# Kernel tuning notes

Measured on AMD Instinct MI355X. Metric: run time of the kernel, lower is better.

## Reference

```python
import jax, jax.numpy as jnp
import numpy as np

B, DIM, D_IN, HID, N_HID_EXTRA = 65536, 128, 64, 512, 2  # num_hidden_layers=3 -> 2 extra hidden linears
LOG_SCALE_CLAMP = 2.0


def _mlp(x, Win, bin_, Whid, bhid, Wout, bout):
    # torch nn.Linear: y = x @ W.T + b
    h = jax.nn.relu(x @ Win.T + bin_)
    for i in range(Whid.shape[0]):  # fixed small layer loop
        h = jax.nn.relu(h @ Whid[i].T + bhid[i])
    return h @ Wout.T + bout


def setup_inputs() -> dict:
    key = jax.random.key(0)
    ks = jax.random.split(key, 13)
    w = lambda k, shp: (jax.random.normal(k, shp, dtype=jnp.float32) * 0.05)
    d_out = DIM - D_IN
    return {
        "z": jax.random.normal(ks[0], (B, DIM), dtype=jnp.float32),
        "s_Win": w(ks[1], (HID, D_IN)),   "s_bin": jnp.zeros((HID,), jnp.float32),
        "s_Whid": w(ks[2], (N_HID_EXTRA, HID, HID)), "s_bhid": jnp.zeros((N_HID_EXTRA, HID), jnp.float32),
        "s_Wout": w(ks[3], (d_out, HID)), "s_bout": jnp.zeros((d_out,), jnp.float32),
        "t_Win": w(ks[4], (HID, D_IN)),   "t_bin": jnp.zeros((HID,), jnp.float32),
        "t_Whid": w(ks[5], (N_HID_EXTRA, HID, HID)), "t_bhid": jnp.zeros((N_HID_EXTRA, HID), jnp.float32),
        "t_Wout": w(ks[6], (d_out, HID)), "t_bout": jnp.zeros((d_out,), jnp.float32),
    }


def reference(z, s_Win, s_bin, s_Whid, s_bhid, s_Wout, s_bout,
              t_Win, t_bin, t_Whid, t_bhid, t_Wout, t_bout):
    # mask = first D_IN dims -> gather reduces to slicing
    z1 = z[:, :D_IN]   # (B, d_in)  passthrough half
    z2 = z[:, D_IN:]   # (B, d_out) transformed half
    log_s = jnp.clip(_mlp(z1, s_Win, s_bin, s_Whid, s_bhid, s_Wout, s_bout),
                     -LOG_SCALE_CLAMP, LOG_SCALE_CLAMP)
    t = _mlp(z1, t_Win, t_bin, t_Whid, t_bhid, t_Wout, t_bout)
    z2_out = z2 * jnp.exp(log_s) + t
    z_out = jnp.concatenate([z1, z2_out], axis=1)  # scatter back per mask
    log_det = log_s.sum(axis=-1)                   # (B,)
    return (z_out, log_det)
```

## Files before the change

kernel.cpp:

```cpp
#include <hip/hip_runtime.h>
#include <stdint.h>


#define NROWS 65536
#define RPB   128
#define NBLK  (NROWS / RPB)

#define OFF_S_WIN   0
#define OFF_S_WHID  32768
#define OFF_S_WOUT  557056
#define OFF_T_WIN   589824
#define OFF_T_WHID  622592
#define OFF_T_WOUT  1146880
#define W_ELEMS     1179648

typedef __attribute__((ext_vector_type(8)))  short short8;
typedef __attribute__((ext_vector_type(4)))  float f32x4;
typedef __attribute__((ext_vector_type(16))) float f32x16;

__device__ __forceinline__ uint32_t f2bf1(float f) {
  uint32_t u = __float_as_uint(f);
  return (u + 0x7fffu + ((u >> 16) & 1u)) >> 16;
}
__device__ __forceinline__ uint32_t pk2bf(float a, float b) {
  return f2bf1(a) | (f2bf1(b) << 16);
}

__global__ void cvt_weights(const float* __restrict__ sWin, const float* __restrict__ sWhid,
                            const float* __restrict__ sWout, const float* __restrict__ tWin,
                            const float* __restrict__ tWhid, const float* __restrict__ tWout,
                            uint16_t* __restrict__ wbf) {
  int g = blockIdx.x * blockDim.x + threadIdx.x;
  int e = g * 4;
  if (e >= W_ELEMS) return;
  const float* src; int off, base; bool k64;
  if      (e < OFF_S_WHID) { src = sWin;  off = e;              base = OFF_S_WIN;  k64 = true; }
  else if (e < OFF_S_WOUT) { src = sWhid; off = e - OFF_S_WHID; base = OFF_S_WHID; k64 = false; }
  else if (e < OFF_T_WIN)  { src = sWout; off = e - OFF_S_WOUT; base = OFF_S_WOUT; k64 = false; }
  else if (e < OFF_T_WHID) { src = tWin;  off = e - OFF_T_WIN;  base = OFF_T_WIN;  k64 = true; }
  else if (e < OFF_T_WOUT) { src = tWhid; off = e - OFF_T_WHID; base = OFF_T_WHID; k64 = false; }
  else                     { src = tWout; off = e - OFF_T_WOUT; base = OFF_T_WOUT; k64 = false; }
  int m, k, tsz;
  if (k64) { m = off >> 6; k = off & 63;  tsz = 2048;  }
  else     { m = off >> 9; k = off & 511; tsz = 16384; }
  int dest = base + (m >> 5) * tsz + (k >> 3) * 256 + (m & 31) * 8 + (k & 7);
  f32x4 v = *(const f32x4*)(src + off);
  uint2 r; r.x = pk2bf(v.x, v.y); r.y = pk2bf(v.z, v.w);
  *(uint2*)(wbf + dest) = r;
}

template<bool BF>
__device__ __forceinline__ short8 ldW(const uint16_t* __restrict__ wb,
                                      const float* __restrict__ wf, int pidx, int oidx) {
  if (BF) {
    return *(const short8*)(wb + pidx);
  } else {
    f32x4 x = *(const f32x4*)(wf + oidx);
    f32x4 y = *(const f32x4*)(wf + oidx + 4);
    short8 r;
    r[0] = (short)f2bf1(x.x); r[1] = (short)f2bf1(x.y);
    r[2] = (short)f2bf1(x.z); r[3] = (short)f2bf1(x.w);
    r[4] = (short)f2bf1(y.x); r[5] = (short)f2bf1(y.y);
    r[6] = (short)f2bf1(y.z); r[7] = (short)f2bf1(y.w);
    return r;
  }
}

#define MFMA32(a, b, c) __builtin_amdgcn_mfma_f32_32x32x16_bf16(a, b, c, 0, 0, 0)

__device__ __forceinline__ void store_h32(f32x16 acc[2][4], const float* __restrict__ bias,
                                          uint16_t* hdst, int wave, int lane) {
  const int l31 = lane & 31, lh = lane >> 5;
  __syncthreads();
  char* wp = (char*)hdst + wave * 16384 + l31 * 16 + lh * 8;
  #pragma unroll
  for (int nt = 0; nt < 2; ++nt) {
    #pragma unroll
    for (int q = 0; q < 4; ++q) {
      const int m0 = wave * 64 + nt * 32 + q * 8 + lh * 4;
      f32x4 bv = *(const f32x4*)(bias + m0);
      #pragma unroll
      for (int rt = 0; rt < 4; ++rt) {
        float v0 = acc[nt][rt][q * 4 + 0] + bv.x;
        float v1 = acc[nt][rt][q * 4 + 1] + bv.y;
        float v2 = acc[nt][rt][q * 4 + 2] + bv.z;
        float v3 = acc[nt][rt][q * 4 + 3] + bv.w;
        uint2 p;
        p.x = pk2bf(fmaxf(v0, 0.f), fmaxf(v1, 0.f));
        p.y = pk2bf(fmaxf(v2, 0.f), fmaxf(v3, 0.f));
        *(uint2*)(wp + nt * 8192 + q * 2048 + rt * 512) = p;
      }
    }
  }
  __syncthreads();
}

template<bool BF>
__device__ __forceinline__ void dense_in(
    const uint16_t* __restrict__ wb, const float* __restrict__ wf,
    const float* __restrict__ bias, const float* __restrict__ z, long rowbase,
    uint16_t* hdst, int wave, int lane) {
  const int l31 = lane & 31, lh = lane >> 5;
  f32x16 acc[2][4];
  #pragma unroll
  for (int i = 0; i < 2; ++i)
    #pragma unroll
    for (int j = 0; j < 4; ++j) acc[i][j] = (f32x16)0.f;
  #pragma unroll 1
  for (int ks = 0; ks < 4; ++ks) {
    short8 a0 = ldW<BF>(wb, wf, (wave * 2 + 0) * 2048 + (2 * ks + lh) * 256 + l31 * 8,
                        (wave * 64 + 0 + l31) * 64 + ks * 16 + lh * 8);
    short8 a1 = ldW<BF>(wb, wf, (wave * 2 + 1) * 2048 + (2 * ks + lh) * 256 + l31 * 8,
                        (wave * 64 + 32 + l31) * 64 + ks * 16 + lh * 8);
    #pragma unroll
    for (int rt = 0; rt < 4; ++rt) {
      const float* zp = z + (rowbase + rt * 32 + l31) * 128 + ks * 16 + lh * 8;
      f32x4 u = *(const f32x4*)zp;
      f32x4 v = *(const f32x4*)(zp + 4);
      short8 b;
      b[0] = (short)f2bf1(u.x); b[1] = (short)f2bf1(u.y);
      b[2] = (short)f2bf1(u.z); b[3] = (short)f2bf1(u.w);
      b[4] = (short)f2bf1(v.x); b[5] = (short)f2bf1(v.y);
      b[6] = (short)f2bf1(v.z); b[7] = (short)f2bf1(v.w);
      acc[0][rt] = MFMA32(a0, b, acc[0][rt]);
      acc[1][rt] = MFMA32(a1, b, acc[1][rt]);
    }
  }
  store_h32(acc, bias, hdst, wave, lane);
}

#define HSTEP(AC0, AC1, BC0, BC1, BC2, BC3, AN0, AN1, BN0, BN1, BN2, BN3, AOFF, BOFF) \
  AN0 = ldW<BF>(wb, wf, wpc + (AOFF),         woc + (AOFF) / 32);                     \
  AN1 = ldW<BF>(wb, wf, wpc + 16384 + (AOFF), woc + 16384 + (AOFF) / 32);             \
  BN0 = *(const short8*)(bc + (BOFF));                                                \
  BN1 = *(const short8*)(bc + (BOFF) + 512);                                          \
  BN2 = *(const short8*)(bc + (BOFF) + 1024);                                         \
  BN3 = *(const short8*)(bc + (BOFF) + 1536);                                         \
  __builtin_amdgcn_s_setprio(1);                                                      \
  acc[0][0] = MFMA32(AC0, BC0, acc[0][0]);                                            \
  acc[0][1] = MFMA32(AC0, BC1, acc[0][1]);                                            \
  acc[0][2] = MFMA32(AC0, BC2, acc[0][2]);                                            \
  acc[0][3] = MFMA32(AC0, BC3, acc[0][3]);                                            \
  acc[1][0] = MFMA32(AC1, BC0, acc[1][0]);                                            \
  acc[1][1] = MFMA32(AC1, BC1, acc[1][1]);                                            \
  acc[1][2] = MFMA32(AC1, BC2, acc[1][2]);                                            \
  acc[1][3] = MFMA32(AC1, BC3, acc[1][3]);                                            \
  __builtin_amdgcn_s_setprio(0);

template<bool BF>
__device__ __forceinline__ void dense_relu512(
    const uint16_t* __restrict__ wb, const float* __restrict__ wf,
    const float* __restrict__ bias, uint16_t* hbuf, int wave, int lane) {
  const int l31 = lane & 31, lh = lane >> 5;
  f32x16 acc[2][4];
  #pragma unroll
  for (int i = 0; i < 2; ++i)
    #pragma unroll
    for (int j = 0; j < 4; ++j) acc[i][j] = (f32x16)0.f;
  const int wbaseP = wave * 2 * 16384 + lh * 256 + l31 * 8;
  const int wbaseO = (wave * 64 + l31) * 512 + lh * 8;
  const char* bb = (const char*)hbuf + lh * 2048 + l31 * 16;

  short8 aC0, aC1, aN0, aN1, bC0, bC1, bC2, bC3, bN0, bN1, bN2, bN3;
  aC0 = ldW<BF>(wb, wf, wbaseP, wbaseO);
  aC1 = ldW<BF>(wb, wf, wbaseP + 16384, wbaseO + 16384);
  bC0 = *(const short8*)(bb);
  bC1 = *(const short8*)(bb + 512);
  bC2 = *(const short8*)(bb + 1024);
  bC3 = *(const short8*)(bb + 1536);

  #pragma unroll 1
  for (int c = 0; c < 7; ++c) {
    const int   wpc = wbaseP + c * 2048;
    const int   woc = wbaseO + c * 64;
    const char* bc  = bb + c * 16384;
    HSTEP(aC0, aC1, bC0, bC1, bC2, bC3, aN0, aN1, bN0, bN1, bN2, bN3, 1 * 512, 1 * 4096)
    HSTEP(aN0, aN1, bN0, bN1, bN2, bN3, aC0, aC1, bC0, bC1, bC2, bC3, 2 * 512, 2 * 4096)
    HSTEP(aC0, aC1, bC0, bC1, bC2, bC3, aN0, aN1, bN0, bN1, bN2, bN3, 3 * 512, 3 * 4096)
    HSTEP(aN0, aN1, bN0, bN1, bN2, bN3, aC0, aC1, bC0, bC1, bC2, bC3, 4 * 512, 4 * 4096)
  }
  {
    const int   wpc = wbaseP + 7 * 2048;
    const int   woc = wbaseO + 7 * 64;
    const char* bc  = bb + 7 * 16384;
    HSTEP(aC0, aC1, bC0, bC1, bC2, bC3, aN0, aN1, bN0, bN1, bN2, bN3, 1 * 512, 1 * 4096)
    HSTEP(aN0, aN1, bN0, bN1, bN2, bN3, aC0, aC1, bC0, bC1, bC2, bC3, 2 * 512, 2 * 4096)
    HSTEP(aC0, aC1, bC0, bC1, bC2, bC3, aN0, aN1, bN0, bN1, bN2, bN3, 3 * 512, 3 * 4096)
    HSTEP(aN0, aN1, bN0, bN1, bN2, bN3, aC0, aC1, bC0, bC1, bC2, bC3, 3 * 512, 4 * 4096)
  }
  store_h32(acc, bias, hbuf, wave, lane);
}

template<bool BF>
__device__ __forceinline__ void final_partial(
    const uint16_t* __restrict__ wb, const float* __restrict__ wf,
    const uint16_t* hbuf, int frt, int fkh, int lane, f32x16 fa[2]) {
  const int l31 = lane & 31, lh = lane >> 5;
  fa[0] = (f32x16)0.f; fa[1] = (f32x16)0.f;
  const int aP = fkh * 8192 + lh * 256 + l31 * 8;
  const int aO = l31 * 512 + fkh * 256 + lh * 8;
  const char* fb = (const char*)hbuf + fkh * 65536 + lh * 2048 + (frt * 32 + l31) * 16;
  #pragma unroll 1
  for (int c = 0; c < 4; ++c) {
    #pragma unroll
    for (int j = 0; j < 4; ++j) {
      const int ks = c * 4 + j;
      short8 b  = *(const short8*)(fb + ks * 4096);
      short8 a0 = ldW<BF>(wb, wf, aP + ks * 512,         aO + ks * 16);
      short8 a1 = ldW<BF>(wb, wf, aP + 16384 + ks * 512, aO + 16384 + ks * 16);
      fa[0] = MFMA32(a0, b, fa[0]);
      fa[1] = MFMA32(a1, b, fa[1]);
    }
  }
}

template<bool BF>
__global__ __launch_bounds__(512, 2) void coupling(
    const float* __restrict__ z,
    const float* __restrict__ sWin, const float* __restrict__ sbin,
    const float* __restrict__ sWhid, const float* __restrict__ sbhid,
    const float* __restrict__ sWout, const float* __restrict__ sbout,
    const float* __restrict__ tWin, const float* __restrict__ tbin,
    const float* __restrict__ tWhid, const float* __restrict__ tbhid,
    const float* __restrict__ tWout, const float* __restrict__ tbout,
    const uint16_t* __restrict__ wbf, float* __restrict__ out) {
  extern __shared__ __align__(16) uint16_t h[];
  const int tid = threadIdx.x;
  const int wave = tid >> 6, lane = tid & 63;
  const int l31 = lane & 31, lh = lane >> 5;
  const long rowbase = (long)blockIdx.x * RPB;
  const int frt = wave & 3, fkh = wave >> 2;

  dense_in<BF>(wbf + OFF_S_WIN, sWin, sbin, z, rowbase, h, wave, lane);
  dense_relu512<BF>(wbf + OFF_S_WHID, sWhid, sbhid, h, wave, lane);
  dense_relu512<BF>(wbf + OFF_S_WHID + 262144, sWhid + 262144, sbhid + 512, h, wave, lane);

  #pragma unroll
  for (int i = 0; i < 4; ++i) {
    int v = tid + i * 512;
    int row = v >> 4, kc = (v & 15) * 4;
    *(f32x4*)(out + (rowbase + row) * 128 + kc) =
        *(const f32x4*)(z + (rowbase + row) * 128 + kc);
  }

  {
    f32x16 fa[2];
    final_partial<BF>(wbf + OFF_S_WOUT, sWout, h, frt, fkh, lane, fa);
    __syncthreads();
    char* sc = (char*)h + frt * 8192 + lane * 128;
    if (fkh) {
      #pragma unroll
      for (int nt = 0; nt < 2; ++nt)
        #pragma unroll
        for (int q = 0; q < 4; ++q)
          *(f32x4*)(sc + nt * 64 + q * 16) =
              (f32x4){fa[nt][q * 4], fa[nt][q * 4 + 1], fa[nt][q * 4 + 2], fa[nt][q * 4 + 3]};
    }
    __syncthreads();
    if (!fkh) {
      const long row = rowbase + frt * 32 + l31;
      float sum = 0.f;
      #pragma unroll
      for (int nt = 0; nt < 2; ++nt) {
        #pragma unroll
        for (int q = 0; q < 4; ++q) {
          f32x4 p = *(const f32x4*)(sc + nt * 64 + q * 16);
          const int m0 = nt * 32 + q * 8 + lh * 4;
          f32x4 bv = *(const f32x4*)(sbout + m0);
          f32x4 v;
          v.x = fminf(fmaxf(fa[nt][q * 4 + 0] + p.x + bv.x, -2.f), 2.f);
          v.y = fminf(fmaxf(fa[nt][q * 4 + 1] + p.y + bv.y, -2.f), 2.f);
          v.z = fminf(fmaxf(fa[nt][q * 4 + 2] + p.z + bv.z, -2.f), 2.f);
          v.w = fminf(fmaxf(fa[nt][q * 4 + 3] + p.w + bv.w, -2.f), 2.f);
          sum += v.x + v.y + v.z + v.w;
          *(f32x4*)(out + row * 128 + 64 + m0) = v;
        }
      }
      sum += __shfl_xor(sum, 32, 64);
      if (lane < 32) out[(long)NROWS * 128 + row] = sum;
    }
  }
  __syncthreads();

  dense_in<BF>(wbf + OFF_T_WIN, tWin, tbin, z, rowbase, h, wave, lane);
  dense_relu512<BF>(wbf + OFF_T_WHID, tWhid, tbhid, h, wave, lane);
  dense_relu512<BF>(wbf + OFF_T_WHID + 262144, tWhid + 262144, tbhid + 512, h, wave, lane);

  {
    f32x16 fa[2];
    final_partial<BF>(wbf + OFF_T_WOUT, tWout, h, frt, fkh, lane, fa);
    __syncthreads();
    char* sc = (char*)h + frt * 8192 + lane * 128;
    if (fkh) {
      #pragma unroll
      for (int nt = 0; nt < 2; ++nt)
        #pragma unroll
        for (int q = 0; q < 4; ++q)
          *(f32x4*)(sc + nt * 64 + q * 16) =
              (f32x4){fa[nt][q * 4], fa[nt][q * 4 + 1], fa[nt][q * 4 + 2], fa[nt][q * 4 + 3]};
    }
    __syncthreads();
    if (!fkh) {
      const long row = rowbase + frt * 32 + l31;
      #pragma unroll
      for (int nt = 0; nt < 2; ++nt) {
        #pragma unroll
        for (int q = 0; q < 4; ++q) {
          f32x4 p = *(const f32x4*)(sc + nt * 64 + q * 16);
          const int m0 = nt * 32 + q * 8 + lh * 4;
          f32x4 bv = *(const f32x4*)(tbout + m0);
          f32x4 tv;
          tv.x = fa[nt][q * 4 + 0] + p.x + bv.x;
          tv.y = fa[nt][q * 4 + 1] + p.y + bv.y;
          tv.z = fa[nt][q * 4 + 2] + p.z + bv.z;
          tv.w = fa[nt][q * 4 + 3] + p.w + bv.w;
          const long o = row * 128 + 64 + m0;
          f32x4 ls = *(const f32x4*)(out + o);
          f32x4 z2 = *(const f32x4*)(z + o);
          f32x4 r;
          r.x = z2.x * __expf(ls.x) + tv.x;
          r.y = z2.y * __expf(ls.y) + tv.y;
          r.z = z2.z * __expf(ls.z) + tv.z;
          r.w = z2.w * __expf(ls.w) + tv.w;
          *(f32x4*)(out + o) = r;
        }
      }
    }
  }
}

extern "C" void kernel_launch(void* const* d_in, const int* in_sizes, int n_in,
                              void* d_out, int out_size, void* d_ws, size_t ws_size,
                              hipStream_t stream) {
  const float* z     = (const float*)d_in[0];
  const float* sWin  = (const float*)d_in[1];
  const float* sbin  = (const float*)d_in[2];
  const float* sWhid = (const float*)d_in[3];
  const float* sbhid = (const float*)d_in[4];
  const float* sWout = (const float*)d_in[5];
  const float* sbout = (const float*)d_in[6];
  const float* tWin  = (const float*)d_in[7];
  const float* tbin  = (const float*)d_in[8];
  const float* tWhid = (const float*)d_in[9];
  const float* tbhid = (const float*)d_in[10];
  const float* tWout = (const float*)d_in[11];
  const float* tbout = (const float*)d_in[12];
  float* out = (float*)d_out;
  const size_t lds_bytes = 139264;

  if (ws_size >= (size_t)W_ELEMS * sizeof(uint16_t)) {
    uint16_t* wbf = (uint16_t*)d_ws;
    cvt_weights<<<W_ELEMS / 4 / 256, 256, 0, stream>>>(sWin, sWhid, sWout, tWin, tWhid, tWout, wbf);
    coupling<true><<<NBLK, 512, lds_bytes, stream>>>(z, sWin, sbin, sWhid, sbhid, sWout, sbout,
                                                     tWin, tbin, tWhid, tbhid, tWout, tbout, wbf, out);
  } else {
    coupling<false><<<NBLK, 512, lds_bytes, stream>>>(z, sWin, sbin, sWhid, sbhid, sWout, sbout,
                                                      tWin, tbin, tWhid, tbhid, tWout, tbout,
                                                      (const uint16_t*)d_in[1], out);
  }
}
```

Before: 194.5 us.

## Stage hidden-layer weights through double-buffered LDS via async global-to-LDS loads

The bf16 weight layout is rewritten so each 16-wide K chunk is stored contiguously. In the 512x512 hidden layers, weights are no longer streamed into registers with a software-pipelined HSTEP macro. Instead, each K chunk is copied asynchronously from global memory into a double-buffered LDS region with global_load_lds, and MFMA operands are read from LDS. This adds a __syncthreads per K step (32 per layer) and shrinks LDS use from 139264 to 163840 bytes? no—uses 65536+16384 elements, trading register prefetching for barrier overhead.

```diff
diff --git a/kernel.cpp b/kernel.cpp
--- a/kernel.cpp
+++ b/kernel.cpp
@@ -14,6 +14,9 @@
 #define OFF_T_WOUT  1146880
 #define W_ELEMS     1179648
 
+#define H_ELEMS     65536
+#define WBUF_ELEMS  8192
+
 typedef __attribute__((ext_vector_type(8)))  short short8;
 typedef __attribute__((ext_vector_type(4)))  float f32x4;
 typedef __attribute__((ext_vector_type(16))) float f32x16;
@@ -24,6 +27,12 @@
 }
 __device__ __forceinline__ uint32_t pk2bf(float a, float b) {
   return f2bf1(a) | (f2bf1(b) << 16);
+}
+
+__device__ __forceinline__ void gl2lds16(const uint16_t* g, uint16_t* l) {
+  __builtin_amdgcn_global_load_lds(
+      (const __attribute__((address_space(1))) uint32_t*)g,
+      (__attribute__((address_space(3))) uint32_t*)l, 16, 0, 0);
 }
 
 __global__ void cvt_weights(const float* __restrict__ sWin, const float* __restrict__ sWhid,
@@ -33,37 +42,34 @@
   int g = blockIdx.x * blockDim.x + threadIdx.x;
   int e = g * 4;
   if (e >= W_ELEMS) return;
-  const float* src; int off, base; bool k64;
-  if      (e < OFF_S_WHID) { src = sWin;  off = e;              base = OFF_S_WIN;  k64 = true; }
-  else if (e < OFF_S_WOUT) { src = sWhid; off = e - OFF_S_WHID; base = OFF_S_WHID; k64 = false; }
-  else if (e < OFF_T_WIN)  { src = sWout; off = e - OFF_S_WOUT; base = OFF_S_WOUT; k64 = false; }
-  else if (e < OFF_T_WHID) { src = tWin;  off = e - OFF_T_WIN;  base = OFF_T_WIN;  k64 = true; }
-  else if (e < OFF_T_WOUT) { src = tWhid; off = e - OFF_T_WHID; base = OFF_T_WHID; k64 = false; }
-  else                     { src = tWout; off = e - OFF_T_WOUT; base = OFF_T_WOUT; k64 = false; }
-  int m, k, tsz;
-  if (k64) { m = off >> 6; k = off & 63;  tsz = 2048;  }
-  else     { m = off >> 9; k = off & 511; tsz = 16384; }
-  int dest = base + (m >> 5) * tsz + (k >> 3) * 256 + (m & 31) * 8 + (k & 7);
+  const float* src; int off, base; int kind;
+  if      (e < OFF_S_WHID) { src = sWin;  off = e;              base = OFF_S_WIN;  kind = 0; }
+  else if (e < OFF_S_WOUT) { src = sWhid; off = e - OFF_S_WHID; base = OFF_S_WHID; kind = 1; }
+  else if (e < OFF_T_WIN)  { src = sWout; off = e - OFF_S_WOUT; base = OFF_S_WOUT; kind = 2; }
+  else if (e < OFF_T_WHID) { src = tWin;  off = e - OFF_T_WIN;  base = OFF_T_WIN;  kind = 0; }
+  else if (e < OFF_T_WOUT) { src = tWhid; off = e - OFF_T_WHID; base = OFF_T_WHID; kind = 1; }
+  else                     { src = tWout; off = e - OFF_T_WOUT; base = OFF_T_WOUT; kind = 2; }
+  int m, k, CH, lay = 0, laysz = 0;
+  if (kind == 0)      { m = off >> 6; k = off & 63;  CH = 8192; }
+  else if (kind == 1) { lay = off >> 18; int o2 = off & 262143;
+                        m = o2 >> 9; k = o2 & 511; CH = 8192; laysz = 262144; }
+  else                { m = off >> 9; k = off & 511; CH = 1024; }
+  int slot = (m & 31) + 32 * ((k >> 3) & 1);
+  int dest = base + lay * laysz + (k >> 4) * CH + (m >> 5) * 512 + slot * 8 + (k & 7);
   f32x4 v = *(const f32x4*)(src + off);
   uint2 r; r.x = pk2bf(v.x, v.y); r.y = pk2bf(v.z, v.w);
   *(uint2*)(wbf + dest) = r;
 }
 
-template<bool BF>
-__device__ __forceinline__ short8 ldW(const uint16_t* __restrict__ wb,
-                                      const float* __restrict__ wf, int pidx, int oidx) {
-  if (BF) {
-    return *(const short8*)(wb + pidx);
-  } else {
-    f32x4 x = *(const f32x4*)(wf + oidx);
-    f32x4 y = *(const f32x4*)(wf + oidx + 4);
-    short8 r;
-    r[0] = (short)f2bf1(x.x); r[1] = (short)f2bf1(x.y);
-    r[2] = (short)f2bf1(x.z); r[3] = (short)f2bf1(x.w);
-    r[4] = (short)f2bf1(y.x); r[5] = (short)f2bf1(y.y);
-    r[6] = (short)f2bf1(y.z); r[7] = (short)f2bf1(y.w);
-    return r;
-  }
+__device__ __forceinline__ short8 ldWf32(const float* __restrict__ wf, int oidx) {
+  f32x4 x = *(const f32x4*)(wf + oidx);
+  f32x4 y = *(const f32x4*)(wf + oidx + 4);
+  short8 r;
+  r[0] = (short)f2bf1(x.x); r[1] = (short)f2bf1(x.y);
+  r[2] = (short)f2bf1(x.z); r[3] = (short)f2bf1(x.w);
+  r[4] = (short)f2bf1(y.x); r[5] = (short)f2bf1(y.y);
+  r[6] = (short)f2bf1(y.z); r[7] = (short)f2bf1(y.w);
+  return r;
 }
 
 #define MFMA32(a, b, c) __builtin_amdgcn_mfma_f32_32x32x16_bf16(a, b, c, 0, 0, 0)
@@ -108,10 +114,14 @@
     for (int j = 0; j < 4; ++j) acc[i][j] = (f32x16)0.f;
   #pragma unroll 1
   for (int ks = 0; ks < 4; ++ks) {
-    short8 a0 = ldW<BF>(wb, wf, (wave * 2 + 0) * 2048 + (2 * ks + lh) * 256 + l31 * 8,
-                        (wave * 64 + 0 + l31) * 64 + ks * 16 + lh * 8);
-    short8 a1 = ldW<BF>(wb, wf, (wave * 2 + 1) * 2048 + (2 * ks + lh) * 256 + l31 * 8,
-                        (wave * 64 + 32 + l31) * 64 + ks * 16 + lh * 8);
+    short8 a0, a1;
+    if (BF) {
+      a0 = *(const short8*)(wb + ks * 8192 + (wave * 2 + 0) * 512 + lane * 8);
+      a1 = *(const short8*)(wb + ks * 8192 + (wave * 2 + 1) * 512 + lane * 8);
+    } else {
+      a0 = ldWf32(wf, (wave * 64 + 0 + l31) * 64 + ks * 16 + lh * 8);
+      a1 = ldWf32(wf, (wave * 64 + 32 + l31) * 64 + ks * 16 + lh * 8);
+    }
     #pragma unroll
     for (int rt = 0; rt < 4; ++rt) {
       const float* zp = z + (rowbase + rt * 32 + l31) * 128 + ks * 16 + lh * 8;
@@ -129,64 +139,56 @@
   store_h32(acc, bias, hdst, wave, lane);
 }
 
-#define HSTEP(AC0, AC1, BC0, BC1, BC2, BC3, AN0, AN1, BN0, BN1, BN2, BN3, AOFF, BOFF) \
-  AN0 = ldW<BF>(wb, wf, wpc + (AOFF),         woc + (AOFF) / 32);                     \
-  AN1 = ldW<BF>(wb, wf, wpc + 16384 + (AOFF), woc + 16384 + (AOFF) / 32);             \
-  BN0 = *(const short8*)(bc + (BOFF));                                                \
-  BN1 = *(const short8*)(bc + (BOFF) + 512);                                          \
-  BN2 = *(const short8*)(bc + (BOFF) + 1024);                                         \
-  BN3 = *(const short8*)(bc + (BOFF) + 1536);                                         \
-  __builtin_amdgcn_s_setprio(1);                                                      \
-  acc[0][0] = MFMA32(AC0, BC0, acc[0][0]);                                            \
-  acc[0][1] = MFMA32(AC0, BC1, acc[0][1]);                                            \
-  acc[0][2] = MFMA32(AC0, BC2, acc[0][2]);                                            \
-  acc[0][3] = MFMA32(AC0, BC3, acc[0][3]);                                            \
-  acc[1][0] = MFMA32(AC1, BC0, acc[1][0]);                                            \
-  acc[1][1] = MFMA32(AC1, BC1, acc[1][1]);                                            \
-  acc[1][2] = MFMA32(AC1, BC2, acc[1][2]);                                            \
-  acc[1][3] = MFMA32(AC1, BC3, acc[1][3]);                                            \
-  __builtin_amdgcn_s_setprio(0);
-
 template<bool BF>
 __device__ __forceinline__ void dense_relu512(
     const uint16_t* __restrict__ wb, const float* __restrict__ wf,
-    const float* __restrict__ bias, uint16_t* hbuf, int wave, int lane) {
+    const float* __restrict__ bias, uint16_t* hbuf, uint16_t* wbuf,
+    int wave, int lane) {
   const int l31 = lane & 31, lh = lane >> 5;
   f32x16 acc[2][4];
   #pragma unroll
   for (int i = 0; i < 2; ++i)
     #pragma unroll
     for (int j = 0; j < 4; ++j) acc[i][j] = (f32x16)0.f;
-  const int wbaseP = wave * 2 * 16384 + lh * 256 + l31 * 8;
-  const int wbaseO = (wave * 64 + l31) * 512 + lh * 8;
   const char* bb = (const char*)hbuf + lh * 2048 + l31 * 16;
 
-  short8 aC0, aC1, aN0, aN1, bC0, bC1, bC2, bC3, bN0, bN1, bN2, bN3;
-  aC0 = ldW<BF>(wb, wf, wbaseP, wbaseO);
-  aC1 = ldW<BF>(wb, wf, wbaseP + 16384, wbaseO + 16384);
-  bC0 = *(const short8*)(bb);
-  bC1 = *(const short8*)(bb + 512);
-  bC2 = *(const short8*)(bb + 1024);
-  bC3 = *(const short8*)(bb + 1536);
+  if (BF) {
+    gl2lds16(wb + (wave * 2 + 0) * 512 + lane * 8, wbuf + (wave * 2 + 0) * 512);
+    gl2lds16(wb + (wave * 2 + 1) * 512 + lane * 8, wbuf + (wave * 2 + 1) * 512);
+  }
 
   #pragma unroll 1
-  for (int c = 0; c < 7; ++c) {
-    const int   wpc = wbaseP + c * 2048;
-    const int   woc = wbaseO + c * 64;
-    const char* bc  = bb + c * 16384;
-    HSTEP(aC0, aC1, bC0, bC1, bC2, bC3, aN0, aN1, bN0, bN1, bN2, bN3, 1 * 512, 1 * 4096)
-    HSTEP(aN0, aN1, bN0, bN1, bN2, bN3, aC0, aC1, bC0, bC1, bC2, bC3, 2 * 512, 2 * 4096)
-    HSTEP(aC0, aC1, bC0, bC1, bC2, bC3, aN0, aN1, bN0, bN1, bN2, bN3, 3 * 512, 3 * 4096)
-    HSTEP(aN0, aN1, bN0, bN1, bN2, bN3, aC0, aC1, bC0, bC1, bC2, bC3, 4 * 512, 4 * 4096)
-  }
-  {
-    const int   wpc = wbaseP + 7 * 2048;
-    const int   woc = wbaseO + 7 * 64;
-    const char* bc  = bb + 7 * 16384;
-    HSTEP(aC0, aC1, bC0, bC1, bC2, bC3, aN0, aN1, bN0, bN1, bN2, bN3, 1 * 512, 1 * 4096)
-    HSTEP(aN0, aN1, bN0, bN1, bN2, bN3, aC0, aC1, bC0, bC1, bC2, bC3, 2 * 512, 2 * 4096)
-    HSTEP(aC0, aC1, bC0, bC1, bC2, bC3, aN0, aN1, bN0, bN1, bN2, bN3, 3 * 512, 3 * 4096)
-    HSTEP(aN0, aN1, bN0, bN1, bN2, bN3, aC0, aC1, bC0, bC1, bC2, bC3, 3 * 512, 4 * 4096)
+  for (int c = 0; c < 32; ++c) {
+    __syncthreads();
+    if (BF && c < 31) {
+      const uint16_t* s = wb + (c + 1) * 8192;
+      uint16_t* d = wbuf + ((c + 1) & 1) * WBUF_ELEMS;
+      gl2lds16(s + (wave * 2 + 0) * 512 + lane * 8, d + (wave * 2 + 0) * 512);
+      gl2lds16(s + (wave * 2 + 1) * 512 + lane * 8, d + (wave * 2 + 1) * 512);
+    }
+    short8 a0, a1;
+    if (BF) {
+      const char* ab = (const char*)(wbuf + (c & 1) * WBUF_ELEMS) + lane * 16;
+      a0 = *(const short8*)(ab + (wave * 2 + 0) * 1024);
+      a1 = *(const short8*)(ab + (wave * 2 + 1) * 1024);
+    } else {
+      a0 = ldWf32(wf, (wave * 64 + 0 + l31) * 512 + c * 16 + lh * 8);
+      a1 = ldWf32(wf, (wave * 64 + 32 + l31) * 512 + c * 16 + lh * 8);
+    }
+    short8 b0 = *(const short8*)(bb + c * 4096);
+    short8 b1 = *(const short8*)(bb + c * 4096 + 512);
+    short8 b2 = *(const short8*)(bb + c * 4096 + 1024);
+    short8 b3 = *(const short8*)(bb + c * 4096 + 1536);
+    __builtin_amdgcn_s_setprio(1);
+    acc[0][0] = MFMA32(a0, b0, acc[0][0]);
+    acc[0][1] = MFMA32(a0, b1, acc[0][1]);
+    acc[0][2] = MFMA32(a0, b2, acc[0][2]);
+    acc[0][3] = MFMA32(a0, b3, acc[0][3]);
+    acc[1][0] = MFMA32(a1, b0, acc[1][0]);
+    acc[1][1] = MFMA32(a1, b1, acc[1][1]);
+    acc[1][2] = MFMA32(a1, b2, acc[1][2]);
+    acc[1][3] = MFMA32(a1, b3, acc[1][3]);
+    __builtin_amdgcn_s_setprio(0);
   }
   store_h32(acc, bias, hbuf, wave, lane);
 }
@@ -197,17 +199,22 @@
     const uint16_t* hbuf, int frt, int fkh, int lane, f32x16 fa[2]) {
   const int l31 = lane & 31, lh = lane >> 5;
   fa[0] = (f32x16)0.f; fa[1] = (f32x16)0.f;
-  const int aP = fkh * 8192 + lh * 256 + l31 * 8;
-  const int aO = l31 * 512 + fkh * 256 + lh * 8;
   const char* fb = (const char*)hbuf + fkh * 65536 + lh * 2048 + (frt * 32 + l31) * 16;
   #pragma unroll 1
-  for (int c = 0; c < 4; ++c) {
+  for (int cc = 0; cc < 4; ++cc) {
     #pragma unroll
     for (int j = 0; j < 4; ++j) {
-      const int ks = c * 4 + j;
-      short8 b  = *(const short8*)(fb + ks * 4096);
-      short8 a0 = ldW<BF>(wb, wf, aP + ks * 512,         aO + ks * 16);
-      short8 a1 = ldW<BF>(wb, wf, aP + 16384 + ks * 512, aO + 16384 + ks * 16);
+      const int ks = cc * 4 + j;
+      const int c = fkh * 16 + ks;
+      short8 b = *(const short8*)(fb + ks * 4096);
+      short8 a0, a1;
+      if (BF) {
+        a0 = *(const short8*)(wb + c * 1024 + lane * 8);
+        a1 = *(const short8*)(wb + c * 1024 + 512 + lane * 8);
+      } else {
+        a0 = ldWf32(wf, (0 + l31) * 512 + c * 16 + lh * 8);
+        a1 = ldWf32(wf, (32 + l31) * 512 + c * 16 + lh * 8);
+      }
       fa[0] = MFMA32(a0, b, fa[0]);
       fa[1] = MFMA32(a1, b, fa[1]);
     }
@@ -225,6 +232,7 @@
     const float* __restrict__ tWout, const float* __restrict__ tbout,
     const uint16_t* __restrict__ wbf, float* __restrict__ out) {
   extern __shared__ __align__(16) uint16_t h[];
+  uint16_t* wbuf = h + H_ELEMS;
   const int tid = threadIdx.x;
   const int wave = tid >> 6, lane = tid & 63;
   const int l31 = lane & 31, lh = lane >> 5;
@@ -232,8 +240,8 @@
   const int frt = wave & 3, fkh = wave >> 2;
 
   dense_in<BF>(wbf + OFF_S_WIN, sWin, sbin, z, rowbase, h, wave, lane);
-  dense_relu512<BF>(wbf + OFF_S_WHID, sWhid, sbhid, h, wave, lane);
-  dense_relu512<BF>(wbf + OFF_S_WHID + 262144, sWhid + 262144, sbhid + 512, h, wave, lane);
+  dense_relu512<BF>(wbf + OFF_S_WHID, sWhid, sbhid, h, wbuf, wave, lane);
+  dense_relu512<BF>(wbf + OFF_S_WHID + 262144, sWhid + 262144, sbhid + 512, h, wbuf, wave, lane);
 
   #pragma unroll
   for (int i = 0; i < 4; ++i) {
@@ -283,8 +291,8 @@
   __syncthreads();
 
   dense_in<BF>(wbf + OFF_T_WIN, tWin, tbin, z, rowbase, h, wave, lane);
-  dense_relu512<BF>(wbf + OFF_T_WHID, tWhid, tbhid, h, wave, lane);
-  dense_relu512<BF>(wbf + OFF_T_WHID + 262144, tWhid + 262144, tbhid + 512, h, wave, lane);
+  dense_relu512<BF>(wbf + OFF_T_WHID, tWhid, tbhid, h, wbuf, wave, lane);
+  dense_relu512<BF>(wbf + OFF_T_WHID + 262144, tWhid + 262144, tbhid + 512, h, wbuf, wave, lane);
 
   {
     f32x16 fa[2];
@@ -346,7 +354,7 @@
   const float* tWout = (const float*)d_in[11];
   const float* tbout = (const float*)d_in[12];
   float* out = (float*)d_out;
-  const size_t lds_bytes = 139264;
+  const size_t lds_bytes = (size_t)(H_ELEMS + 2 * WBUF_ELEMS) * sizeof(uint16_t);
 
   if (ws_size >= (size_t)W_ELEMS * sizeof(uint16_t)) {
     uint16_t* wbf = (uint16_t*)d_ws;
```

Result: slower. 227.1 us (+16.8%).
